# Optimization experiments

Hardware: AMD Instinct MI355X
Metric: run time of the kernel (lower is better)

Reference implementation:

```python
import jax, jax.numpy as jnp
import numpy as np

N = 50000      # nodes
E = 1600000    # edges per graph
IN = 64
HID = 64
OUT = 64


def _gat_conv(x, edge_index, W, a_src, a_dst, bias):
    """PyG GATConv, heads=1, add_self_loops=True, negative_slope=0.2."""
    n = x.shape[0]
    h = x @ W                                   # [N, d]
    loop = jnp.arange(n, dtype=edge_index.dtype)
    src = jnp.concatenate([edge_index[0], loop])
    dst = jnp.concatenate([edge_index[1], loop])
    e = jax.nn.leaky_relu((h @ a_src)[src] + (h @ a_dst)[dst], negative_slope=0.2)
    m = jax.ops.segment_max(e, dst, num_segments=n)          # stable edge-softmax per dst
    w = jnp.exp(e - m[dst])
    denom = jax.ops.segment_sum(w, dst, num_segments=n)
    alpha = w / denom[dst]                                   # [E+N]
    out = jax.ops.segment_sum(h[src] * alpha[:, None], dst, num_segments=n)
    return out + bias


def setup_inputs() -> dict:
    key = jax.random.key(0)
    ks = jax.random.split(key, 32)

    def glorot(k, shape):
        fan_out = shape[1] if len(shape) > 1 else 1
        lim = (6.0 / (shape[0] + fan_out)) ** 0.5
        return jax.random.uniform(k, shape, minval=-lim, maxval=lim, dtype=jnp.float32)

    inp = {
        "x_ind": jax.random.normal(ks[0], (N, IN), jnp.float32),
        "x_pos": jax.random.normal(ks[1], (N, IN), jnp.float32),
        "edge_ind": jax.random.randint(ks[2], (2, E), 0, N, dtype=jnp.int32),
        "edge_pos": jax.random.randint(ks[3], (2, E), 0, N, dtype=jnp.int32),
        "w1_ind": glorot(ks[4], (IN, HID)),
        "as1_ind": glorot(ks[5], (HID,)),
        "ad1_ind": glorot(ks[6], (HID,)),
        "b1_ind": jnp.zeros((HID,), jnp.float32),
        "w2_ind": glorot(ks[7], (HID, OUT)),
        "as2_ind": glorot(ks[8], (OUT,)),
        "ad2_ind": glorot(ks[9], (OUT,)),
        "b2_ind": jnp.zeros((OUT,), jnp.float32),
        "w1_pos": glorot(ks[10], (IN, HID)),
        "as1_pos": glorot(ks[11], (HID,)),
        "ad1_pos": glorot(ks[12], (HID,)),
        "b1_pos": jnp.zeros((HID,), jnp.float32),
        "w2_pos": glorot(ks[13], (HID, OUT)),
        "as2_pos": glorot(ks[14], (OUT,)),
        "ad2_pos": glorot(ks[15], (OUT,)),
        "b2_pos": jnp.zeros((OUT,), jnp.float32),
        "first_hop_att": glorot(ks[16], (2, HID)),
        "att_weight": glorot(ks[17], (2, OUT)),
        "mlp_w": glorot(ks[18], (OUT, 1)),
        "mlp_b": jnp.zeros((1,), jnp.float32),
    }
    return inp


def reference(x_ind, x_pos, edge_ind, edge_pos,
              w1_ind, as1_ind, ad1_ind, b1_ind,
              w2_ind, as2_ind, ad2_ind, b2_ind,
              w1_pos, as1_pos, ad1_pos, b1_pos,
              w2_pos, as2_pos, ad2_pos, b2_pos,
              first_hop_att, att_weight, mlp_w, mlp_b):
    h_i = jax.nn.relu(_gat_conv(x_ind, edge_ind, w1_ind, as1_ind, ad1_ind, b1_ind))
    h_p = jax.nn.relu(_gat_conv(x_pos, edge_pos, w1_pos, as1_pos, ad1_pos, b1_pos))
    # first-hop branch attention over the two graphs
    s1 = jnp.stack([jnp.sum(first_hop_att[0] * h_i, axis=1),
                    jnp.sum(first_hop_att[1] * h_p, axis=1)], axis=0)  # [2, N]
    a1 = jax.nn.softmax(s1, axis=0)
    fused = a1[0][:, None] * h_i + a1[1][:, None] * h_p
    g_i = _gat_conv(fused, edge_ind, w2_ind, as2_ind, ad2_ind, b2_ind)
    g_p = _gat_conv(fused, edge_pos, w2_pos, as2_pos, ad2_pos, b2_pos)
    s2 = jnp.stack([jnp.sum(att_weight[0] * g_i, axis=1),
                    jnp.sum(att_weight[1] * g_p, axis=1)], axis=0)
    a2 = jax.nn.softmax(s2, axis=0)
    x = a2[0][:, None] * g_i + a2[1][:, None] * g_p
    return x @ mlp_w + mlp_b                    # [N, 1]
```

## Files before the change

kernel.cpp:

```cpp
#include <hip/hip_runtime.h>
#include <hip/hip_fp16.h>

#define ND 64
#define BG 128
#define MAXB 1024
#define PCH 16384
#define CAP 4608

__device__ __forceinline__ float lrelu(float x) { return x > 0.f ? x : 0.2f * x; }

__device__ __forceinline__ float wave_sum(float v) {
#pragma unroll
    for (int m = 32; m > 0; m >>= 1) v += __shfl_xor(v, m, 64);
    return v;
}

__device__ __forceinline__ void fma8(float* acc, float w, int4 raw) {
    union { int4 i; __half h[8]; } u;
    u.i = raw;
#pragma unroll
    for (int i = 0; i < 8; i++) acc[i] = fmaf(w, __half2float(u.h[i]), acc[i]);
}


__device__ void partition_body(int* hist, int* lcur,
                               const int* __restrict__ eI, const int* __restrict__ eP,
                               int* __restrict__ bcursor, int* __restrict__ part,
                               int N, int E, int nb) {
    int t = threadIdx.x;
    int total = 2 * E;
    int chunkBase = blockIdx.x * PCH;
    int cnt = min(PCH, total - chunkBase);
    if (t < nb) hist[t] = 0;
    __syncthreads();

    if (cnt == PCH) {
        int pk[16];
        unsigned bkp[8];
#pragma unroll
        for (int it = 0; it < 4; it++) {
            int i = t * 4 + it * 4096;
            int e = chunkBase + i;
            int sv[4], dv[4];
            if (e + 3 < E) {
                int4 a = *(const int4*)(eI + e);
                int4 b = *(const int4*)(eI + E + e);
                sv[0] = a.x; sv[1] = a.y; sv[2] = a.z; sv[3] = a.w;
                dv[0] = b.x; dv[1] = b.y; dv[2] = b.z; dv[3] = b.w;
            } else if (e >= E) {
                int4 a = *(const int4*)(eP + (e - E));
                int4 b = *(const int4*)(eP + E + (e - E));
                sv[0] = a.x; sv[1] = a.y; sv[2] = a.z; sv[3] = a.w;
                dv[0] = b.x + N; dv[1] = b.y + N; dv[2] = b.z + N; dv[3] = b.w + N;
            } else {
#pragma unroll
                for (int k = 0; k < 4; k++) {
                    int ee = e + k;
                    if (ee < E) { sv[k] = eI[ee]; dv[k] = eI[E + ee]; }
                    else        { sv[k] = eP[ee - E]; dv[k] = N + eP[E + ee - E]; }
                }
            }
#pragma unroll
            for (int k = 0; k < 4; k++) {
                int j = it * 4 + k;
                int bk = dv[k] >> 7;
                pk[j] = (sv[k] << 8) | (dv[k] & 255);
                atomicAdd(&hist[bk], 1);
                if ((j & 1) == 0) bkp[j >> 1] = (unsigned)bk;
                else bkp[j >> 1] |= (unsigned)bk << 16;
            }
        }
        __syncthreads();
        if (t < nb) lcur[t] = t * CAP + (hist[t] ? atomicAdd(&bcursor[t], hist[t]) : 0);
        __syncthreads();
#pragma unroll
        for (int j = 0; j < 16; j++) {
            int bk = (bkp[j >> 1] >> ((j & 1) * 16)) & 0xffff;
            int pos = atomicAdd(&lcur[bk], 1);
            part[pos] = pk[j];
        }
        return;
    }

    int cnt4 = cnt & ~3;
    for (int i = t * 4; i < cnt4; i += 4096) {
        int e = chunkBase + i;
        int4 d; int base;
        if (e + 3 < E)   { d = *(const int4*)(eI + E + e); base = 0; }
        else if (e >= E) { d = *(const int4*)(eP + E + (e - E)); base = N; }
        else {
            int tmp[4];
#pragma unroll
            for (int k = 0; k < 4; k++) {
                int ee = e + k;
                tmp[k] = (ee < E) ? eI[E + ee] : N + eP[E + ee - E];
            }
            d = make_int4(tmp[0], tmp[1], tmp[2], tmp[3]); base = 0;
        }
        atomicAdd(&hist[(base + d.x) >> 7], 1);
        atomicAdd(&hist[(base + d.y) >> 7], 1);
        atomicAdd(&hist[(base + d.z) >> 7], 1);
        atomicAdd(&hist[(base + d.w) >> 7], 1);
    }
    for (int i = cnt4 + t; i < cnt; i += 1024) {
        int e = chunkBase + i;
        int idx = (e < E) ? eI[E + e] : N + eP[E + (e - E)];
        atomicAdd(&hist[idx >> 7], 1);
    }
    __syncthreads();
    if (t < nb) lcur[t] = t * CAP + (hist[t] ? atomicAdd(&bcursor[t], hist[t]) : 0);
    __syncthreads();
    for (int i = t; i < cnt; i += 1024) {
        int e = chunkBase + i;
        int s, idx;
        if (e < E) { s = eI[e]; idx = eI[E + e]; }
        else       { s = eP[e - E]; idx = N + eP[E + (e - E)]; }
        int pos = atomicAdd(&lcur[idx >> 7], 1);
        part[pos] = (s << 8) | (idx & 255);
    }
}

__device__ void gemm_body(float* xsAll, int gb,
                          const float* __restrict__ xA, const float* __restrict__ xB,
                          const float* __restrict__ WA, const float* __restrict__ WB,
                          const float* __restrict__ asA, const float* __restrict__ adA,
                          const float* __restrict__ asB, const float* __restrict__ adB,
                          __half* __restrict__ h16, float* __restrict__ ssrc,
                          float* __restrict__ sdst, int N) {
    int half = gb & 1;
    int blk = gb >> 1;
    int wave = threadIdx.x >> 6;
    int lane = threadIdx.x & 63;
    const float* x  = half ? xB : xA;
    const float* W  = half ? WB : WA;
    const float* av_ = half ? asB : asA;
    const float* dv_ = half ? adB : adA;
    int nodeBase = (blk * 16 + wave) * 4;
    float* xs = xsAll + wave * (4 * ND);

    if (nodeBase + 3 < N) {
        *(float4*)&xs[lane * 4] = *(const float4*)&x[(size_t)nodeBase * ND + lane * 4];
    } else if (nodeBase < N) {
#pragma unroll
        for (int i = 0; i < 4; i++) {
            int gi = nodeBase * ND + lane * 4 + i;
            xs[lane * 4 + i] = (gi < N * ND) ? x[gi] : 0.f;
        }
    }
    __syncthreads();
    if (nodeBase >= N) return;

    float4 acc = {0.f, 0.f, 0.f, 0.f};
#pragma unroll
    for (int k = 0; k < ND; k++) {
        float wv = W[k * ND + lane];
        acc.x = fmaf(xs[0 * ND + k], wv, acc.x);
        acc.y = fmaf(xs[1 * ND + k], wv, acc.y);
        acc.z = fmaf(xs[2 * ND + k], wv, acc.z);
        acc.w = fmaf(xs[3 * ND + k], wv, acc.w);
    }
    float av = av_[lane], dv = dv_[lane];
    float s1x = wave_sum(acc.x * av), s2x = wave_sum(acc.x * dv);
    float s1y = wave_sum(acc.y * av), s2y = wave_sum(acc.y * dv);
    float s1z = wave_sum(acc.z * av), s2z = wave_sum(acc.z * dv);
    float s1w = wave_sum(acc.w * av), s2w = wave_sum(acc.w * dv);

    int g0 = half * N + nodeBase;
    h16[(size_t)(g0 + 0) * ND + lane] = __float2half(acc.x);
    if (nodeBase + 1 < N) h16[(size_t)(g0 + 1) * ND + lane] = __float2half(acc.y);
    if (nodeBase + 2 < N) h16[(size_t)(g0 + 2) * ND + lane] = __float2half(acc.z);
    if (nodeBase + 3 < N) h16[(size_t)(g0 + 3) * ND + lane] = __float2half(acc.w);
    if (lane == 0) {
        ssrc[g0] = s1x; sdst[g0] = s2x;
        if (nodeBase + 1 < N) { ssrc[g0 + 1] = s1y; sdst[g0 + 1] = s2y; }
        if (nodeBase + 2 < N) { ssrc[g0 + 2] = s1z; sdst[g0 + 2] = s2z; }
        if (nodeBase + 3 < N) { ssrc[g0 + 3] = s1w; sdst[g0 + 3] = s2w; }
    }
}

__global__ void __launch_bounds__(1024) part_gemm(
        const int* __restrict__ eI, const int* __restrict__ eP,
        int* __restrict__ bcursor, int* __restrict__ part,
        const float* __restrict__ xA, const float* __restrict__ xB,
        const float* __restrict__ WA, const float* __restrict__ WB,
        const float* __restrict__ asA, const float* __restrict__ adA,
        const float* __restrict__ asB, const float* __restrict__ adB,
        __half* __restrict__ h16, float* __restrict__ ssrc, float* __restrict__ sdst,
        int N, int E, int nb, int partBlocks) {
    __shared__ int smem[16 * 4 * ND];
    if (blockIdx.x < partBlocks) {
        partition_body(smem, smem + MAXB, eI, eP, bcursor, part, N, E, nb);
    } else {
        gemm_body((float*)smem, blockIdx.x - partBlocks,
                  xA, xB, WA, WB, asA, adA, asB, adB, h16, ssrc, sdst, N);
    }
}

__global__ void bucket_build(const int* __restrict__ part, const int* __restrict__ bcursor,
                             int* __restrict__ row, int* __restrict__ deg,
                             int* __restrict__ csr, int n2, int N) {
    __shared__ int lhist[BG * 8];
    __shared__ int lrow[BG * 8];
    __shared__ int slab[CAP];
    __shared__ int wsum[16];
    int b = blockIdx.x, t = threadIdx.x;
    int lane = t & 63, wave = t >> 6;
    int start = b * CAP;
    int cnt = min(bcursor[b], CAP);
    int cnt4 = cnt & ~3;
    int t1 = (N * 1) >> 3, t2 = (N * 2) >> 3, t3 = (N * 3) >> 3, t4 = (N * 4) >> 3;
    int t5 = (N * 5) >> 3, t6 = (N * 6) >> 3, t7 = (N * 7) >> 3;
    auto key = [&](int p) {
        int s = p >> 8;
        int o = (s >= t1) + (s >= t2) + (s >= t3) + (s >= t4)
              + (s >= t5) + (s >= t6) + (s >= t7);
        return ((p & 127) << 3) | o;
    };
    lhist[t] = 0;
    __syncthreads();
    for (int j = t * 4; j < cnt4; j += 4096) {
        int4 p = *(const int4*)(part + start + j);
        atomicAdd(&lhist[key(p.x)], 1);
        atomicAdd(&lhist[key(p.y)], 1);
        atomicAdd(&lhist[key(p.z)], 1);
        atomicAdd(&lhist[key(p.w)], 1);
    }
    for (int j = cnt4 + t; j < cnt; j += 1024) atomicAdd(&lhist[key(part[start + j])], 1);
    __syncthreads();
    int v = lhist[t];
    int ws = v;
#pragma unroll
    for (int m = 1; m < 64; m <<= 1) {
        int up = __shfl_up(ws, m, 64);
        if (lane >= m) ws += up;
    }
    if (lane == 63) wsum[wave] = ws;
    __syncthreads();
    if (t < 16) {
        int x = wsum[t];
#pragma unroll
        for (int m = 1; m < 16; m <<= 1) {
            int up = __shfl_up(x, m, 16);
            if ((t & 15) >= m) x += up;
        }
        wsum[t] = x;
    }
    __syncthreads();
    int incl = ws + (wave ? wsum[wave - 1] : 0);
    lrow[t] = incl;
    __syncthreads();
    if (t < BG) {
        int g = b * BG + t;
        if (g < n2) {
            row[g] = start + lrow[8 * t] - lhist[8 * t];
            int d = 0;
#pragma unroll
            for (int i = 0; i < 8; i++) d += lhist[8 * t + i];
            deg[g] = d;
        }
    }
    __syncthreads();
    lhist[t] = incl - v;
    __syncthreads();
    for (int j = t * 4; j < cnt4; j += 4096) {
        int4 p = *(const int4*)(part + start + j);
        int pos;
        pos = atomicAdd(&lhist[key(p.x)], 1); slab[pos] = p.x >> 8;
        pos = atomicAdd(&lhist[key(p.y)], 1); slab[pos] = p.y >> 8;
        pos = atomicAdd(&lhist[key(p.z)], 1); slab[pos] = p.z >> 8;
        pos = atomicAdd(&lhist[key(p.w)], 1); slab[pos] = p.w >> 8;
    }
    for (int j = cnt4 + t; j < cnt; j += 1024) {
        int p = part[start + j];
        int pos = atomicAdd(&lhist[key(p)], 1);
        slab[pos] = p >> 8;
    }
    __syncthreads();
    {
        int ge = incl, gs = ge - v;
        for (int i = gs + 1; i < ge; i++) {
            int x = slab[i], j2 = i - 1;
            while (j2 >= gs && slab[j2] > x) { slab[j2 + 1] = slab[j2]; j2--; }
            slab[j2 + 1] = x;
        }
    }
    __syncthreads();
    for (int j = t * 4; j < cnt4; j += 4096)
        *(int4*)(csr + start + j) = *(const int4*)(slab + j);
    for (int j = cnt4 + t; j < cnt; j += 1024) csr[start + j] = slab[j];
}


__device__ __forceinline__ void gather_body(
        const int* __restrict__ csr, int start, int cnt, float sd,
        const float* __restrict__ ss, const __half* __restrict__ hh,
        int l16, int slot, int fl8, int waveBase,
        float* acc, float& denomp) {
    int c16 = min(16, cnt);
    int sj = (l16 < c16) ? csr[start + l16] : 0;
    float wj = (l16 < c16) ? __expf(lrelu(ss[sj] + sd)) : 0.f;

    for (int base = 0; base < cnt; base += 16) {
        int nb2 = base + 16;
        int sjn = 0; float svn = 0.f; int c16n = cnt - nb2;
        if (nb2 < cnt) {
            sjn = (l16 < c16n) ? csr[start + nb2 + l16] : 0;
            svn = (l16 < c16n) ? ss[sjn] : 0.f;
        }
        denomp += wj;
        int nq = (min(16, cnt - base) + 1) >> 1;
        float w0 = __shfl(wj, waveBase + slot, 64);
        int s0 = __shfl(sj, waveBase + slot, 64);
        int4 r0 = *(const int4*)(hh + (size_t)s0 * ND + fl8);
        if (nq > 1) {
            float w1 = __shfl(wj, waveBase + 2 + slot, 64);
            int s1 = __shfl(sj, waveBase + 2 + slot, 64);
            int4 r1 = *(const int4*)(hh + (size_t)s1 * ND + fl8);
            for (int c = 2; c < nq; c++) {
                float w2 = __shfl(wj, waveBase + c * 2 + slot, 64);
                int s2 = __shfl(sj, waveBase + c * 2 + slot, 64);
                int4 r2 = *(const int4*)(hh + (size_t)s2 * ND + fl8);
                fma8(acc, w0, r0);
                w0 = w1; r0 = r1;
                w1 = w2; r1 = r2;
            }
            fma8(acc, w0, r0);
            fma8(acc, w1, r1);
        } else {
            fma8(acc, w0, r0);
        }
        if (nb2 < cnt) {
            wj = (l16 < c16n) ? __expf(lrelu(svn + sd)) : 0.f;
            sj = sjn;
        }
    }
}

__global__ void agg1_h(const int* __restrict__ csr, const int* __restrict__ row,
                       const int* __restrict__ deg, const float* __restrict__ ss1,
                       const float* __restrict__ sd1, const __half* __restrict__ h16a,
                       const float* __restrict__ bA, const float* __restrict__ bB,
                       const float* __restrict__ fha,
                       __half* __restrict__ h1, float* __restrict__ plog, int N) {
    int half = blockIdx.x & 1;
    int wave = threadIdx.x >> 6;
    int lane = threadIdx.x & 63;
    int sub  = lane >> 4;
    int l16  = lane & 15;
    int slot = l16 >> 3;
    int fl8  = (l16 & 7) * 8;
    int node = ((blockIdx.x >> 1) * 4 + wave) * 4 + sub;
    bool valid = node < N;
    int g = half * N + node;
    const float* bias = half ? bB : bA;
    const float* ss = ss1 + (size_t)half * N;
    const __half* hh = h16a + (size_t)half * N * ND;
    const float* fhah = fha + half * ND;

    int start = valid ? row[g] : 0;
    int cnt   = valid ? deg[g] : 0;
    float sd  = valid ? sd1[g] : 0.f;
    float wself = valid ? __expf(lrelu(ss[node] + sd)) : 0.f;

    float acc[8] = {0.f, 0.f, 0.f, 0.f, 0.f, 0.f, 0.f, 0.f};
    float denomp = 0.f;
    gather_body(csr, start, cnt, sd, ss, hh, l16, slot, fl8, sub << 4, acc, denomp);

#pragma unroll
    for (int i = 0; i < 8; i++) acc[i] += __shfl_xor(acc[i], 8, 64);
#pragma unroll
    for (int m = 1; m <= 8; m <<= 1) denomp += __shfl_xor(denomp, m, 64);
    float denom = denomp + wself;

    if (!valid || slot != 0) return;
    int4 rawS = *(const int4*)(hh + (size_t)node * ND + fl8);
    union { int4 i; __half h[8]; } us;
    us.i = rawS;
    float v[8];
#pragma unroll
    for (int i = 0; i < 8; i++)
        v[i] = fmaxf((acc[i] + wself * __half2float(us.h[i])) / denom + bias[fl8 + i], 0.f);
    union { int4 i; __half h[8]; } uo;
#pragma unroll
    for (int i = 0; i < 8; i++) uo.h[i] = __float2half(v[i]);
    *(int4*)&h1[(size_t)g * ND + fl8] = uo.i;
    float p = 0.f;
#pragma unroll
    for (int i = 0; i < 8; i++) p = fmaf(fhah[fl8 + i], v[i], p);
    p += __shfl_xor(p, 1, 64);
    p += __shfl_xor(p, 2, 64);
    p += __shfl_xor(p, 4, 64);
    if (l16 == 0) plog[g] = p;
}

__global__ void __launch_bounds__(512) gemm2_combine(
        const __half* __restrict__ h1, const float* __restrict__ plog,
        const float* __restrict__ W2A, const float* __restrict__ W2B,
        const float* __restrict__ as2A, const float* __restrict__ ad2A,
        const float* __restrict__ as2B, const float* __restrict__ ad2B,
        __half* __restrict__ h16b, float* __restrict__ ssrc2,
        float* __restrict__ sdst2, int N) {
    __shared__ float xs[16][ND];
    int t = threadIdx.x;
    int n0 = blockIdx.x * 16;
    if (t < 256) {
        int r = t >> 4, c = (t & 15) * 4;
        int n = n0 + r;
        float4 f = make_float4(0.f, 0.f, 0.f, 0.f);
        if (n < N) {
            union { int2 i; __half h[4]; } uI, uP;
            uI.i = *(const int2*)&h1[(size_t)n * ND + c];
            uP.i = *(const int2*)&h1[((size_t)N + n) * ND + c];
            float p0 = plog[n], p1 = plog[N + n];
            float mx = fmaxf(p0, p1);
            float e0 = __expf(p0 - mx), e1 = __expf(p1 - mx);
            float inv = 1.f / (e0 + e1);
            e0 *= inv; e1 *= inv;
            f.x = e0 * __half2float(uI.h[0]) + e1 * __half2float(uP.h[0]);
            f.y = e0 * __half2float(uI.h[1]) + e1 * __half2float(uP.h[1]);
            f.z = e0 * __half2float(uI.h[2]) + e1 * __half2float(uP.h[2]);
            f.w = e0 * __half2float(uI.h[3]) + e1 * __half2float(uP.h[3]);
        }
        *(float4*)&xs[r][c] = f;
    }
    __syncthreads();
    int wave = t >> 6, lane = t & 63;
    int half = wave >> 2;
    int nb0 = (wave & 3) * 4;
    const float* W  = half ? W2B : W2A;
    const float* av_ = half ? as2B : as2A;
    const float* dv_ = half ? ad2B : ad2A;

    float4 acc = {0.f, 0.f, 0.f, 0.f};
#pragma unroll
    for (int k = 0; k < ND; k++) {
        float wv = W[k * ND + lane];
        acc.x = fmaf(xs[nb0 + 0][k], wv, acc.x);
        acc.y = fmaf(xs[nb0 + 1][k], wv, acc.y);
        acc.z = fmaf(xs[nb0 + 2][k], wv, acc.z);
        acc.w = fmaf(xs[nb0 + 3][k], wv, acc.w);
    }
    float av = av_[lane], dv = dv_[lane];
    float s1x = wave_sum(acc.x * av), s2x = wave_sum(acc.x * dv);
    float s1y = wave_sum(acc.y * av), s2y = wave_sum(acc.y * dv);
    float s1z = wave_sum(acc.z * av), s2z = wave_sum(acc.z * dv);
    float s1w = wave_sum(acc.w * av), s2w = wave_sum(acc.w * dv);

    int node = n0 + nb0;
    int g0 = half * N + node;
    if (node + 0 < N) h16b[(size_t)(g0 + 0) * ND + lane] = __float2half(acc.x);
    if (node + 1 < N) h16b[(size_t)(g0 + 1) * ND + lane] = __float2half(acc.y);
    if (node + 2 < N) h16b[(size_t)(g0 + 2) * ND + lane] = __float2half(acc.z);
    if (node + 3 < N) h16b[(size_t)(g0 + 3) * ND + lane] = __float2half(acc.w);
    if (lane == 0) {
        if (node + 0 < N) { ssrc2[g0 + 0] = s1x; sdst2[g0 + 0] = s2x; }
        if (node + 1 < N) { ssrc2[g0 + 1] = s1y; sdst2[g0 + 1] = s2y; }
        if (node + 2 < N) { ssrc2[g0 + 2] = s1z; sdst2[g0 + 2] = s2z; }
        if (node + 3 < N) { ssrc2[g0 + 3] = s1w; sdst2[g0 + 3] = s2w; }
    }
}

__global__ void agg2_dots(const int* __restrict__ csr, const int* __restrict__ row,
                          const int* __restrict__ deg, const float* __restrict__ ss2,
                          const float* __restrict__ sd2, const __half* __restrict__ h16b,
                          const float* __restrict__ bA, const float* __restrict__ bB,
                          const float* __restrict__ attw, const float* __restrict__ mlpw,
                          float* __restrict__ satt, float* __restrict__ mmlp, int N) {
    int half = blockIdx.x & 1;
    int wave = threadIdx.x >> 6;
    int lane = threadIdx.x & 63;
    int sub  = lane >> 4;
    int l16  = lane & 15;
    int slot = l16 >> 3;
    int fl8  = (l16 & 7) * 8;
    int node = ((blockIdx.x >> 1) * 4 + wave) * 4 + sub;
    bool valid = node < N;
    int g = half * N + node;
    const float* bias = half ? bB : bA;
    const float* ss = ss2 + (size_t)half * N;
    const __half* hh = h16b + (size_t)half * N * ND;
    const float* attwh = attw + half * ND;

    int start = valid ? row[g] : 0;
    int cnt   = valid ? deg[g] : 0;
    float sd  = valid ? sd2[g] : 0.f;
    float wself = valid ? __expf(lrelu(ss[node] + sd)) : 0.f;

    float acc[8] = {0.f, 0.f, 0.f, 0.f, 0.f, 0.f, 0.f, 0.f};
    float denomp = 0.f;
    gather_body(csr, start, cnt, sd, ss, hh, l16, slot, fl8, sub << 4, acc, denomp);

#pragma unroll
    for (int i = 0; i < 8; i++) acc[i] += __shfl_xor(acc[i], 8, 64);
#pragma unroll
    for (int m = 1; m <= 8; m <<= 1) denomp += __shfl_xor(denomp, m, 64);
    float denom = denomp + wself;

    if (!valid || slot != 0) return;
    int4 rawS = *(const int4*)(hh + (size_t)node * ND + fl8);
    union { int4 i; __half h[8]; } us;
    us.i = rawS;
    float pa = 0.f, pm = 0.f;
#pragma unroll
    for (int i = 0; i < 8; i++) {
        float vi = (acc[i] + wself * __half2float(us.h[i])) / denom + bias[fl8 + i];
        pa = fmaf(attwh[fl8 + i], vi, pa);
        pm = fmaf(mlpw[fl8 + i], vi, pm);
    }
    pa += __shfl_xor(pa, 1, 64); pm += __shfl_xor(pm, 1, 64);
    pa += __shfl_xor(pa, 2, 64); pm += __shfl_xor(pm, 2, 64);
    pa += __shfl_xor(pa, 4, 64); pm += __shfl_xor(pm, 4, 64);
    if (l16 == 0) { satt[g] = pa; mmlp[g] = pm; }
}

__global__ void final_combine(const float* __restrict__ satt, const float* __restrict__ mmlp,
                              const float* __restrict__ mlpb, float* __restrict__ out, int N) {
    int i = blockIdx.x * blockDim.x + threadIdx.x;
    if (i >= N) return;
    float s0 = satt[i], s1 = satt[N + i];
    float m = fmaxf(s0, s1);
    float e0 = __expf(s0 - m), e1 = __expf(s1 - m);
    out[i] = (e0 * mmlp[i] + e1 * mmlp[N + i]) / (e0 + e1) + mlpb[0];
}

extern "C" void kernel_launch(void* const* d_in, const int* in_sizes, int n_in,
                              void* d_out, int out_size, void* d_ws, size_t ws_size,
                              hipStream_t stream) {
    const int N = in_sizes[0] / ND;
    const int E = in_sizes[2] / 2;

    const float* x_ind = (const float*)d_in[0];
    const float* x_pos = (const float*)d_in[1];
    const int*   e_ind = (const int*)d_in[2];
    const int*   e_pos = (const int*)d_in[3];
    const float* w1i = (const float*)d_in[4];
    const float* as1i = (const float*)d_in[5];
    const float* ad1i = (const float*)d_in[6];
    const float* b1i = (const float*)d_in[7];
    const float* w2i = (const float*)d_in[8];
    const float* as2i = (const float*)d_in[9];
    const float* ad2i = (const float*)d_in[10];
    const float* b2i = (const float*)d_in[11];
    const float* w1p = (const float*)d_in[12];
    const float* as1p = (const float*)d_in[13];
    const float* ad1p = (const float*)d_in[14];
    const float* b1p = (const float*)d_in[15];
    const float* w2p = (const float*)d_in[16];
    const float* as2p = (const float*)d_in[17];
    const float* ad2p = (const float*)d_in[18];
    const float* b2p = (const float*)d_in[19];
    const float* fha = (const float*)d_in[20];
    const float* attw = (const float*)d_in[21];
    const float* mlpw = (const float*)d_in[22];
    const float* mlpb = (const float*)d_in[23];

    char* ws = (char*)d_ws;
    size_t off = 0;
    auto alloc = [&](size_t elems) { void* p = ws + off; off += elems * 4; return p; };

    const int n2 = 2 * N;
    const int nb = (n2 + BG - 1) / BG;

    __half* h16a = (__half*)alloc((size_t)n2 * ND / 2);
    float* ssrc1 = (float*)alloc(n2);
    float* sdst1 = (float*)alloc(n2);
    float* ssrc2 = (float*)alloc(n2);
    float* sdst2 = (float*)alloc(n2);
    float* plog  = (float*)alloc(n2);
    float* satt  = (float*)alloc(n2);
    float* mmlp  = (float*)alloc(n2);
    int* deg    = (int*)alloc(n2);
    int* rowi   = (int*)alloc(n2);
    int* csr    = (int*)alloc((size_t)nb * CAP);
    int* bcursor= (int*)alloc(MAXB);
    int* part   = (int*)alloc((size_t)nb * CAP);
    __half* h1 = (__half*)part;
    __half* h16b = h16a;

    const int partBlocks  = (2 * E + PCH - 1) / PCH;
    const int gemm1Blocks = 2 * ((N + 63) / 64);
    const int aggBlocks   = 2 * ((N + 15) / 16);
    const int gemm2Blocks = (N + 15) / 16;
    const int finBlocks   = (N + 255) / 256;

    hipMemsetAsync(bcursor, 0, MAXB * sizeof(int), stream);
    part_gemm<<<partBlocks + gemm1Blocks, 1024, 0, stream>>>(
        e_ind, e_pos, bcursor, part,
        x_ind, x_pos, w1i, w1p, as1i, ad1i, as1p, ad1p,
        h16a, ssrc1, sdst1, N, E, nb, partBlocks);
    bucket_build<<<nb, 1024, 0, stream>>>(part, bcursor, rowi, deg, csr, n2, N);

    agg1_h<<<aggBlocks, 256, 0, stream>>>(
        csr, rowi, deg, ssrc1, sdst1, h16a, b1i, b1p, fha, h1, plog, N);

    gemm2_combine<<<gemm2Blocks, 512, 0, stream>>>(
        h1, plog, w2i, w2p, as2i, ad2i, as2p, ad2p, h16b, ssrc2, sdst2, N);

    agg2_dots<<<aggBlocks, 256, 0, stream>>>(
        csr, rowi, deg, ssrc2, sdst2, h16b, b2i, b2p, attw, mlpw, satt, mmlp, N);

    final_combine<<<finBlocks, 256, 0, stream>>>(satt, mmlp, mlpb, (float*)d_out, N);
}
```

Before: 326.5 us.

## Project layer-2 features to attention and MLP scalars before edge aggregation

```diff
diff --git a/kernel.cpp b/kernel.cpp
--- a/kernel.cpp
+++ b/kernel.cpp
@@ -398,8 +398,9 @@
         const float* __restrict__ W2A, const float* __restrict__ W2B,
         const float* __restrict__ as2A, const float* __restrict__ ad2A,
         const float* __restrict__ as2B, const float* __restrict__ ad2B,
-        __half* __restrict__ h16b, float* __restrict__ ssrc2,
-        float* __restrict__ sdst2, int N) {
+        const float* __restrict__ attw, const float* __restrict__ mlpw,
+        float* __restrict__ ssrc2, float* __restrict__ sdst2,
+        float* __restrict__ ta, float* __restrict__ tm, int N) {
     __shared__ float xs[16][ND];
     int t = threadIdx.x;
     int n0 = blockIdx.x * 16;
@@ -430,6 +431,7 @@
     const float* W  = half ? W2B : W2A;
     const float* av_ = half ? as2B : as2A;
     const float* dv_ = half ? ad2B : ad2A;
+    const float* awh = attw + half * ND;
 
     float4 acc = {0.f, 0.f, 0.f, 0.f};
 #pragma unroll
@@ -441,29 +443,31 @@
         acc.w = fmaf(xs[nb0 + 3][k], wv, acc.w);
     }
     float av = av_[lane], dv = dv_[lane];
+    float aw = awh[lane], mw = mlpw[lane];
     float s1x = wave_sum(acc.x * av), s2x = wave_sum(acc.x * dv);
     float s1y = wave_sum(acc.y * av), s2y = wave_sum(acc.y * dv);
     float s1z = wave_sum(acc.z * av), s2z = wave_sum(acc.z * dv);
     float s1w = wave_sum(acc.w * av), s2w = wave_sum(acc.w * dv);
+    float tax = wave_sum(acc.x * aw), tmx = wave_sum(acc.x * mw);
+    float tay = wave_sum(acc.y * aw), tmy = wave_sum(acc.y * mw);
+    float taz = wave_sum(acc.z * aw), tmz = wave_sum(acc.z * mw);
+    float taw = wave_sum(acc.w * aw), tmw = wave_sum(acc.w * mw);
 
     int node = n0 + nb0;
     int g0 = half * N + node;
-    if (node + 0 < N) h16b[(size_t)(g0 + 0) * ND + lane] = __float2half(acc.x);
-    if (node + 1 < N) h16b[(size_t)(g0 + 1) * ND + lane] = __float2half(acc.y);
-    if (node + 2 < N) h16b[(size_t)(g0 + 2) * ND + lane] = __float2half(acc.z);
-    if (node + 3 < N) h16b[(size_t)(g0 + 3) * ND + lane] = __float2half(acc.w);
     if (lane == 0) {
-        if (node + 0 < N) { ssrc2[g0 + 0] = s1x; sdst2[g0 + 0] = s2x; }
-        if (node + 1 < N) { ssrc2[g0 + 1] = s1y; sdst2[g0 + 1] = s2y; }
-        if (node + 2 < N) { ssrc2[g0 + 2] = s1z; sdst2[g0 + 2] = s2z; }
-        if (node + 3 < N) { ssrc2[g0 + 3] = s1w; sdst2[g0 + 3] = s2w; }
-    }
-}
-
-__global__ void agg2_dots(const int* __restrict__ csr, const int* __restrict__ row,
+        if (node + 0 < N) { ssrc2[g0 + 0] = s1x; sdst2[g0 + 0] = s2x; ta[g0 + 0] = tax; tm[g0 + 0] = tmx; }
+        if (node + 1 < N) { ssrc2[g0 + 1] = s1y; sdst2[g0 + 1] = s2y; ta[g0 + 1] = tay; tm[g0 + 1] = tmy; }
+        if (node + 2 < N) { ssrc2[g0 + 2] = s1z; sdst2[g0 + 2] = s2z; ta[g0 + 2] = taz; tm[g0 + 2] = tmz; }
+        if (node + 3 < N) { ssrc2[g0 + 3] = s1w; sdst2[g0 + 3] = s2w; ta[g0 + 3] = taw; tm[g0 + 3] = tmw; }
+    }
+}
+
+__global__ void agg2_scal(const int* __restrict__ csr, const int* __restrict__ row,
                           const int* __restrict__ deg, const float* __restrict__ ss2,
-                          const float* __restrict__ sd2, const __half* __restrict__ h16b,
-                          const float* __restrict__ bA, const float* __restrict__ bB,
+                          const float* __restrict__ sd2,
+                          const float* __restrict__ ta, const float* __restrict__ tm,
+                          const float* __restrict__ b2A, const float* __restrict__ b2B,
                           const float* __restrict__ attw, const float* __restrict__ mlpw,
                           float* __restrict__ satt, float* __restrict__ mmlp, int N) {
     int half = blockIdx.x & 1;
@@ -471,46 +475,41 @@
     int lane = threadIdx.x & 63;
     int sub  = lane >> 4;
     int l16  = lane & 15;
-    int slot = l16 >> 3;
-    int fl8  = (l16 & 7) * 8;
     int node = ((blockIdx.x >> 1) * 4 + wave) * 4 + sub;
     bool valid = node < N;
     int g = half * N + node;
-    const float* bias = half ? bB : bA;
     const float* ss = ss2 + (size_t)half * N;
-    const __half* hh = h16b + (size_t)half * N * ND;
-    const float* attwh = attw + half * ND;
+    const float* tah = ta + (size_t)half * N;
+    const float* tmh = tm + (size_t)half * N;
+    const float* bh = half ? b2B : b2A;
+    const float* awh = attw + half * ND;
+
+    float attb = wave_sum(awh[lane] * bh[lane]);
+    float mb   = wave_sum(mlpw[lane] * bh[lane]);
 
     int start = valid ? row[g] : 0;
     int cnt   = valid ? deg[g] : 0;
     float sd  = valid ? sd2[g] : 0.f;
-    float wself = valid ? __expf(lrelu(ss[node] + sd)) : 0.f;
-
-    float acc[8] = {0.f, 0.f, 0.f, 0.f, 0.f, 0.f, 0.f, 0.f};
-    float denomp = 0.f;
-    gather_body(csr, start, cnt, sd, ss, hh, l16, slot, fl8, sub << 4, acc, denomp);
-
-#pragma unroll
-    for (int i = 0; i < 8; i++) acc[i] += __shfl_xor(acc[i], 8, 64);
-#pragma unroll
-    for (int m = 1; m <= 8; m <<= 1) denomp += __shfl_xor(denomp, m, 64);
-    float denom = denomp + wself;
-
-    if (!valid || slot != 0) return;
-    int4 rawS = *(const int4*)(hh + (size_t)node * ND + fl8);
-    union { int4 i; __half h[8]; } us;
-    us.i = rawS;
-    float pa = 0.f, pm = 0.f;
-#pragma unroll
-    for (int i = 0; i < 8; i++) {
-        float vi = (acc[i] + wself * __half2float(us.h[i])) / denom + bias[fl8 + i];
-        pa = fmaf(attwh[fl8 + i], vi, pa);
-        pm = fmaf(mlpw[fl8 + i], vi, pm);
-    }
-    pa += __shfl_xor(pa, 1, 64); pm += __shfl_xor(pm, 1, 64);
-    pa += __shfl_xor(pa, 2, 64); pm += __shfl_xor(pm, 2, 64);
-    pa += __shfl_xor(pa, 4, 64); pm += __shfl_xor(pm, 4, 64);
-    if (l16 == 0) { satt[g] = pa; mmlp[g] = pm; }
+
+    float aw = 0.f, aa = 0.f, am = 0.f;
+    for (int j = l16; j < cnt; j += 16) {
+        int s = csr[start + j];
+        float w = __expf(lrelu(ss[s] + sd));
+        aw += w;
+        aa = fmaf(w, tah[s], aa);
+        am = fmaf(w, tmh[s], am);
+    }
+#pragma unroll
+    for (int m = 1; m <= 8; m <<= 1) {
+        aw += __shfl_xor(aw, m, 64);
+        aa += __shfl_xor(aa, m, 64);
+        am += __shfl_xor(am, m, 64);
+    }
+    if (!valid || l16 != 0) return;
+    float wself = __expf(lrelu(ss[node] + sd));
+    float denom = aw + wself;
+    satt[g] = (aa + wself * tah[node]) / denom + attb;
+    mmlp[g] = (am + wself * tmh[node]) / denom + mb;
 }
 
 __global__ void final_combine(const float* __restrict__ satt, const float* __restrict__ mmlp,
@@ -569,13 +568,14 @@
     float* plog  = (float*)alloc(n2);
     float* satt  = (float*)alloc(n2);
     float* mmlp  = (float*)alloc(n2);
+    float* tad   = (float*)alloc(n2);
+    float* tmd   = (float*)alloc(n2);
     int* deg    = (int*)alloc(n2);
     int* rowi   = (int*)alloc(n2);
     int* csr    = (int*)alloc((size_t)nb * CAP);
     int* bcursor= (int*)alloc(MAXB);
     int* part   = (int*)alloc((size_t)nb * CAP);
     __half* h1 = (__half*)part;
-    __half* h16b = h16a;
 
     const int partBlocks  = (2 * E + PCH - 1) / PCH;
     const int gemm1Blocks = 2 * ((N + 63) / 64);
@@ -594,10 +594,12 @@
         csr, rowi, deg, ssrc1, sdst1, h16a, b1i, b1p, fha, h1, plog, N);
 
     gemm2_combine<<<gemm2Blocks, 512, 0, stream>>>(
-        h1, plog, w2i, w2p, as2i, ad2i, as2p, ad2p, h16b, ssrc2, sdst2, N);
-
-    agg2_dots<<<aggBlocks, 256, 0, stream>>>(
-        csr, rowi, deg, ssrc2, sdst2, h16b, b2i, b2p, attw, mlpw, satt, mmlp, N);
+        h1, plog, w2i, w2p, as2i, ad2i, as2p, ad2p,
+        attw, mlpw, ssrc2, sdst2, tad, tmd, N);
+
+    agg2_scal<<<aggBlocks, 256, 0, stream>>>(
+        csr, rowi, deg, ssrc2, sdst2, tad, tmd, b2i, b2p,
+        attw, mlpw, satt, mmlp, N);
 
     final_combine<<<finBlocks, 256, 0, stream>>>(satt, mmlp, mlpb, (float*)d_out, N);
 }
```

New measurement: 327.9 us. About the same (+0.4%).
